# Optimization experiments

Measured on AMD Instinct MI355X. Metric: run time of the kernel, lower is better.

Reference implementation:

```python
import jax, jax.numpy as jnp
import numpy as np
from jax import lax

LATTICE = (16, 16)          # translation-group shape
N_CELLS = 16 * 16           # 256
N_POINT = 8                 # point-group size (e.g. square-lattice C4v)
N_SYMM = N_POINT * N_CELLS  # 2048
FEATURES = 64
IN_FEATURES = 64
BATCH = 64


def setup_inputs() -> dict:
    key = jax.random.key(0)
    k1, k2, k3, k4 = jax.random.split(key, 4)
    x = jax.random.normal(k1, (BATCH, IN_FEATURES, N_SYMM), dtype=jnp.float32)
    kernel = jax.random.normal(k2, (FEATURES, IN_FEATURES, N_SYMM), dtype=jnp.float32) * (
        1.0 / np.sqrt(IN_FEATURES * N_SYMM)
    )
    bias = jax.random.normal(k3, (FEATURES,), dtype=jnp.float32) * 0.02
    product_table = jax.random.randint(k4, (N_POINT, N_SYMM), 0, N_SYMM, dtype=jnp.int64)
    return {"x": x, "kernel": kernel, "bias": bias, "product_table": product_table}


def reference(x, kernel, bias, product_table):
    batch_shape = x.shape[:-2]
    in_features = x.shape[-2]
    # mapping: pt[:n_point] -> (n_point, n_point, *lattice)
    mapping = (
        product_table.reshape(N_POINT, N_CELLS, N_POINT)
        .transpose(0, 2, 1)
        .reshape(N_POINT, N_POINT, *LATTICE)
    )
    # activations: (..., in_f, n_symm) -> (B, in_f, n_point, *lattice)
    xg = x.reshape(-1, in_features, N_CELLS, N_POINT).transpose(0, 1, 3, 2)
    xg = xg.reshape(*xg.shape[:-1], *LATTICE)
    # equivariant kernel via gather: (feat, in_f, n_point, n_point, *lattice)
    kg = kernel[..., mapping]
    # FFT over the translation lattice
    xf = jnp.fft.fftn(xg, s=LATTICE).reshape(*xg.shape[:3], N_CELLS)       # (B,in_f,np,cells)
    kf = jnp.fft.fftn(kg, s=LATTICE).reshape(*kg.shape[:4], N_CELLS)       # (F,in_f,np,np,cells)
    # batched complex contraction over (in_f, n_point), batch over cells
    y = lax.dot_general(xf, kf, (((1, 2), (1, 2)), ((3,), (4,))))          # (cells,B,F,np)
    y = y.transpose(1, 2, 3, 0)                                            # (B,F,np,cells)
    y = y.reshape(*y.shape[:3], *LATTICE)
    y = jnp.fft.ifftn(y, s=LATTICE).reshape(*y.shape[:3], N_CELLS)
    y = y.transpose(0, 1, 3, 2).reshape(*batch_shape, FEATURES, N_SYMM)
    y = y + bias[:, None]
    # input dtype is float32 -> complex result cannot cast back, return real part
    return y.real.astype(jnp.float32)
```

## Files before the change

### kernel.cpp

```cpp
#include <hip/hip_runtime.h>
#include <hip/hip_bf16.h>

typedef __attribute__((ext_vector_type(8))) short bf16x8;
typedef __attribute__((ext_vector_type(16))) float f32x16;
typedef __attribute__((ext_vector_type(2))) float f32x2;
typedef unsigned short ushort_t;

constexpr int NS  = 2048;
constexpr int F   = 64;
constexpr int IFT = 64;
constexpr int B   = 64;
constexpr int NCS = 144;

constexpr float CT[16] = {
    1.0f,  0.9238795325112867f,  0.7071067811865476f,  0.3826834323650898f,
    0.0f, -0.3826834323650898f, -0.7071067811865476f, -0.9238795325112867f,
   -1.0f, -0.9238795325112867f, -0.7071067811865476f, -0.3826834323650898f,
    0.0f,  0.3826834323650898f,  0.7071067811865476f,  0.9238795325112867f};
constexpr float ST[16] = {
    0.0f,  0.3826834323650898f,  0.7071067811865476f,  0.9238795325112867f,
    1.0f,  0.9238795325112867f,  0.7071067811865476f,  0.3826834323650898f,
    0.0f, -0.3826834323650898f, -0.7071067811865476f, -0.9238795325112867f,
   -1.0f, -0.9238795325112867f, -0.7071067811865476f, -0.3826834323650898f};

constexpr int DR4[16] = {0,4,8,12, 1,5,9,13, 2,6,10,14, 3,7,11,15};

template<bool INV>
__device__ inline void dft4(float& ar, float& ai, float& br, float& bi,
                            float& cr, float& ci, float& dr, float& di)
{
    const float t0r = ar + cr, t0i = ai + ci;
    const float t1r = ar - cr, t1i = ai - ci;
    const float t2r = br + dr, t2i = bi + di;
    const float t3r = br - dr, t3i = bi - di;
    ar = t0r + t2r; ai = t0i + t2i;
    cr = t0r - t2r; ci = t0i - t2i;
    if (!INV) { br = t1r + t3i; bi = t1i - t3r; dr = t1r - t3i; di = t1i + t3r; }
    else      { br = t1r - t3i; bi = t1i + t3r; dr = t1r + t3i; di = t1i - t3r; }
}

template<bool INV>
__device__ inline void fft16(float* xr, float* xi)
{
#pragma unroll
    for (int r = 0; r < 4; ++r)
        dft4<INV>(xr[r], xi[r], xr[r + 4], xi[r + 4],
                  xr[r + 8], xi[r + 8], xr[r + 12], xi[r + 12]);
#pragma unroll
    for (int r = 1; r < 4; ++r)
#pragma unroll
        for (int q = 1; q < 4; ++q) {
            const int t = (r * q) & 15;
            const int s = r + 4 * q;
            if (t == 4) {
                const float tr = xr[s];
                if (!INV) { xr[s] = xi[s];  xi[s] = -tr; }
                else      { xr[s] = -xi[s]; xi[s] = tr;  }
            } else {
                const float c = CT[t], sn = INV ? ST[t] : -ST[t];
                const float tr = xr[s];
                xr[s] = tr * c - xi[s] * sn;
                xi[s] = tr * sn + xi[s] * c;
            }
        }
#pragma unroll
    for (int q = 0; q < 4; ++q)
        dft4<INV>(xr[4 * q], xi[4 * q], xr[4 * q + 1], xi[4 * q + 1],
                  xr[4 * q + 2], xi[4 * q + 2], xr[4 * q + 3], xi[4 * q + 3]);
}

template<bool INV>
__device__ inline void dft4c(f32x2& a, f32x2& b, f32x2& c, f32x2& d)
{
    const f32x2 t0 = a + c, t1 = a - c;
    const f32x2 t2 = b + d, t3 = b - d;
    a = t0 + t2; c = t0 - t2;
    f32x2 jt3;
    if (!INV) { jt3.x = t3.y;  jt3.y = -t3.x; }
    else      { jt3.x = -t3.y; jt3.y = t3.x;  }
    b = t1 + jt3; d = t1 - jt3;
}

template<bool INV>
__device__ inline void fft16c(f32x2* z)
{
#pragma unroll
    for (int r = 0; r < 4; ++r) dft4c<INV>(z[r], z[r + 4], z[r + 8], z[r + 12]);
#pragma unroll
    for (int r = 1; r < 4; ++r)
#pragma unroll
        for (int q = 1; q < 4; ++q) {
            const int t = (r * q) & 15, s = r + 4 * q;
            if (t == 4) {
                const f32x2 v = z[s];
                if (!INV) { z[s].x = v.y;  z[s].y = -v.x; }
                else      { z[s].x = -v.y; z[s].y = v.x;  }
            } else {
                const float c = CT[t], sn = INV ? ST[t] : -ST[t];
                const f32x2 v = z[s];
                f32x2 w;
                w.x = v.x * c - v.y * sn;
                w.y = v.x * sn + v.y * c;
                z[s] = w;
            }
        }
#pragma unroll
    for (int q = 0; q < 4; ++q) dft4c<INV>(z[4 * q], z[4 * q + 1], z[4 * q + 2], z[4 * q + 3]);
}

__device__ inline float bf2f(ushort_t h) { return __uint_as_float(((unsigned)h) << 16); }

__device__ inline unsigned pkbf(float a, float b) {
    union { __hip_bfloat162 h2; unsigned u; } c;
    c.h2 = __float22bfloat162_rn(make_float2(a, b));
    return c.u;
}

__device__ inline bf16x8 bneg(bf16x8 v) {
    union { bf16x8 b; unsigned u[4]; } x; x.b = v;
    x.u[0] ^= 0x80008000u; x.u[1] ^= 0x80008000u;
    x.u[2] ^= 0x80008000u; x.u[3] ^= 0x80008000u;
    return x.b;
}

__global__ __launch_bounds__(256) void permute_pt_kernel(
    const int* __restrict__ pt, int* __restrict__ pt2)
{
    const int t = blockIdx.x * 256 + threadIdx.x;
    const int a = t >> 11, r = t & 2047;
    const int bq = r >> 8, s = r & 255;
    pt2[t] = pt[a * NS + s * 8 + bq];
}

__global__ __launch_bounds__(256, 4) void fft_x_kernel(
    const float* __restrict__ x, ushort_t* __restrict__ xf, int i0, int KB)
{
    __shared__ float t_re[16][152], t_im[16][152];
    __shared__ ushort_t stgx[NCS * 68];
    const int tid = threadIdx.x;
    const int bp = blockIdx.x;
    const int il = blockIdx.y;

    const int g = tid >> 4, l = tid & 15;
    const int bloc = g & 1, a = g >> 1;
    const int b = bp * 2 + bloc;
    const int i = i0 + il;

    const float* xr_g = x + ((size_t)b * IFT + i) * NS;
    float xr[16], xi[16];
#pragma unroll
    for (int sx = 0; sx < 16; ++sx) { xr[sx] = xr_g[(l * 16 + sx) * 8 + a]; xi[sx] = 0.f; }
    fft16<false>(xr, xi);
#pragma unroll
    for (int kx = 0; kx < 9; ++kx) {
        t_re[g][kx * 17 + l] = xr[DR4[kx]];
        t_im[g][kx * 17 + l] = xi[DR4[kx]];
    }
    __syncthreads();

    if (l < 9) {
        float Tr[16], Ti[16];
#pragma unroll
        for (int n = 0; n < 16; ++n) { Tr[n] = t_re[g][l * 17 + n]; Ti[n] = t_im[g][l * 17 + n]; }
        fft16<false>(Tr, Ti);
#pragma unroll
        for (int ky = 0; ky < 16; ++ky) {
            const float sr = Tr[DR4[ky]], si = Ti[DR4[ky]];
            const int cs = ky * 9 + l;
            const unsigned w0 = pkbf(sr, si);
            const float rhf = bf2f((ushort_t)(w0 & 0xffffu));
            const float ihf = bf2f((ushort_t)(w0 >> 16));
            const unsigned w1 = pkbf(sr - rhf, si - ihf);
            *(uint2*)&stgx[cs * 68 + bloc * 32 + a * 4] = make_uint2(w0, w1);
        }
    }
    __syncthreads();

    const int kb = il >> 1, mt = bp >> 4;
    const int lb = (il & 1) * 32 + (bp & 15) * 2;
    const size_t PS = (size_t)NCS * 512;
    for (int t = tid; t < NCS * 8; t += 256) {
        const int cs = t >> 3, v4 = (t >> 1) & 3, h = t & 1;
        const int us = ((v4 & 1) << 1) | (v4 >> 1);
        union { ushort_t s[8]; uint4 u; } tmp;
        const int base = cs * 68 + h * 32 + us;
#pragma unroll
        for (int j = 0; j < 8; ++j) tmp.s[j] = stgx[base + j * 4];
        const size_t off = (size_t)(kb * 8 + mt * 4 + v4) * PS + (size_t)cs * 512 + (size_t)(lb + h) * 8;
        *(uint4*)(xf + off) = tmp.u;
    }
}

__global__ __launch_bounds__(256, 4) void fft_k_kernel(
    const float* __restrict__ kern, const int* __restrict__ pt2,
    ushort_t* __restrict__ kf, int i0, int KB)
{
    __shared__ __align__(16) f32x2 t2[16 * 153];
    __shared__ __align__(16) unsigned stgk[NCS * 18];
    f32x2* krow2 = &t2[0];

    const int tid = threadIdx.x;
    const int fg  = blockIdx.x & 15;
    const int bqp = blockIdx.x >> 4;
    const int il  = blockIdx.y;
    const int i   = i0 + il;

    const int g = tid >> 4, l = tid & 15;
    const int bql = g & 1, a = g >> 1;
    const int bq  = bqp * 2 + bql;

    int idx[16];
    const int4* pp = (const int4*)(pt2 + ((a * 8 + bq) * 256 + l * 16));
#pragma unroll
    for (int q = 0; q < 4; ++q) {
        const int4 t4 = pp[q];
        idx[q * 4] = t4.x; idx[q * 4 + 1] = t4.y; idx[q * 4 + 2] = t4.z; idx[q * 4 + 3] = t4.w;
    }

    const int kb = il >> 1;
    const int nt = fg;
    const int pg = (tid * 57) >> 9;
    const int pl = tid - pg * 9;
    const int slot = (pg & 1) * 8 + (pg >> 1);
    const size_t PS = (size_t)NCS * 512;

    for (int p = 0; p < 2; ++p) {
        const int f0 = fg * 4 + p * 2;
        {
            const float4* s0 = (const float4*)(kern + ((size_t)f0 * IFT + i) * NS);
            const float4* s1 = (const float4*)(kern + ((size_t)(f0 + 1) * IFT + i) * NS);
            for (int u = tid; u < 512; u += 256) {
                const float4 va = s0[u], vb = s1[u];
                float4* dst = (float4*)(krow2 + (size_t)u * 4);
                dst[0] = make_float4(va.x, vb.x, va.y, vb.y);
                dst[1] = make_float4(va.z, vb.z, va.w, vb.w);
            }
        }
        __syncthreads();
        f32x2 z[16];
#pragma unroll
        for (int sx = 0; sx < 16; ++sx) z[sx] = krow2[idx[sx]];
        __syncthreads();

        fft16c<false>(z);
        f32x2 F1[9];
#pragma unroll
        for (int kx = 0; kx < 9; ++kx) {
            const f32x2 Zk = z[DR4[kx]];
            const f32x2 Zm = z[DR4[(16 - kx) & 15]];
            f32x2 F0;
            F0.x = (Zk.x + Zm.x) * 0.5f;
            F0.y = (Zk.y - Zm.y) * 0.5f;
            F1[kx].x = (Zk.y + Zm.y) * 0.5f;
            F1[kx].y = (Zm.x - Zk.x) * 0.5f;
            t2[g * 153 + kx * 17 + l] = F0;
        }

        for (int sub = 0; sub < 2; ++sub) {
            if (sub == 1) {
#pragma unroll
                for (int kx = 0; kx < 9; ++kx) t2[g * 153 + kx * 17 + l] = F1[kx];
            }
            __syncthreads();

            if (tid < 144) {
                f32x2 c[16];
#pragma unroll
                for (int n = 0; n < 16; ++n) c[n] = t2[pg * 153 + pl * 17 + n];
                fft16c<false>(c);
#pragma unroll
                for (int ky = 0; ky < 16; ++ky) {
                    const int cs = ky * 9 + pl;
                    const f32x2 v = c[DR4[ky]];
                    stgk[cs * 18 + slot] = pkbf(v.x, v.y);
                }
            }
            __syncthreads();

            const int f = f0 + sub;
            const int lbase = (il & 1) * 32 + (f & 3) * 8 + bqp * 2;
            for (int t = tid; t < NCS * 2; t += 256) {
                const int cs = t >> 1, h = t & 1;
                const int base = cs * 18 + h * 8;
                unsigned w[8];
                *(uint2*)&w[0] = *(const uint2*)&stgk[base];
                *(uint2*)&w[2] = *(const uint2*)&stgk[base + 2];
                *(uint2*)&w[4] = *(const uint2*)&stgk[base + 4];
                *(uint2*)&w[6] = *(const uint2*)&stgk[base + 6];
                union { ushort_t s[8]; uint4 u; } lo, hi;
#pragma unroll
                for (int j = 0; j < 8; ++j) { lo.s[j] = (ushort_t)(w[j] & 0xffffu); hi.s[j] = (ushort_t)(w[j] >> 16); }
                const size_t off = (size_t)(kb * 32 + nt * 2) * PS + (size_t)cs * 512 + (size_t)(lbase + h) * 8;
                *(uint4*)(kf + off) = lo.u;
                *(uint4*)(kf + off + PS) = hi.u;
            }
            __syncthreads();
        }
    }
}

#define MFMA(acc, A, Bv) acc = __builtin_amdgcn_mfma_f32_32x32x16_bf16(A, Bv, acc, 0, 0, 0)
#define LDB(p) (*(const bf16x8*)(p))

__global__ __launch_bounds__(256) void gemm_kernel(
    const ushort_t* __restrict__ xf, const ushort_t* __restrict__ kf,
    float* __restrict__ yre, float* __restrict__ yim, int KB, int acc)
{
    const int cs = blockIdx.x, nb = blockIdx.y;
    const int w = threadIdx.x >> 6, lane = threadIdx.x & 63;
    const int nt = nb * 4 + w;
    const size_t PS = (size_t)NCS * 512;

    f32x16 cre0, cim0, cre1, cim1;
#pragma unroll
    for (int q = 0; q < 16; ++q) { cre0[q] = 0.f; cim0[q] = 0.f; cre1[q] = 0.f; cim1[q] = 0.f; }

    const ushort_t* ab = xf + (size_t)cs * 512 + (size_t)lane * 8;
    const ushort_t* bb = kf + (size_t)cs * 512 + (size_t)(nt * 2) * PS + (size_t)lane * 8;

    const ushort_t* ap = ab;
    const ushort_t* bp = bb;
    bf16x8 Brh = LDB(bp), Bih = LDB(bp + PS);
    bf16x8 Arh0 = LDB(ap), Arl0 = LDB(ap + PS), Aih0 = LDB(ap + 2 * PS), Ail0 = LDB(ap + 3 * PS);
    bf16x8 Arh1 = LDB(ap + 4 * PS), Arl1 = LDB(ap + 5 * PS), Aih1 = LDB(ap + 6 * PS), Ail1 = LDB(ap + 7 * PS);

    for (int kb = 0; kb < KB; ++kb) {
        const int kn = (kb + 1 < KB) ? kb + 1 : kb;
        const ushort_t* an = ab + (size_t)kn * 8 * PS;
        const ushort_t* bn = bb + (size_t)kn * 32 * PS;
        const bf16x8 nBrh = LDB(bn), nBih = LDB(bn + PS);
        const bf16x8 nArh0 = LDB(an), nArl0 = LDB(an + PS), nAih0 = LDB(an + 2 * PS), nAil0 = LDB(an + 3 * PS);
        const bf16x8 nArh1 = LDB(an + 4 * PS), nArl1 = LDB(an + 5 * PS), nAih1 = LDB(an + 6 * PS), nAil1 = LDB(an + 7 * PS);

        const bf16x8 NAih0 = bneg(Aih0), NAil0 = bneg(Ail0);
        const bf16x8 NAih1 = bneg(Aih1), NAil1 = bneg(Ail1);

        MFMA(cre0, Arh0, Brh); MFMA(cre0, Arl0, Brh);
        MFMA(cre0, NAih0, Bih); MFMA(cre0, NAil0, Bih);
        MFMA(cim0, Arh0, Bih); MFMA(cim0, Arl0, Bih);
        MFMA(cim0, Aih0, Brh); MFMA(cim0, Ail0, Brh);
        MFMA(cre1, Arh1, Brh); MFMA(cre1, Arl1, Brh);
        MFMA(cre1, NAih1, Bih); MFMA(cre1, NAil1, Bih);
        MFMA(cim1, Arh1, Bih); MFMA(cim1, Arl1, Bih);
        MFMA(cim1, Aih1, Brh); MFMA(cim1, Ail1, Brh);

        Brh = nBrh; Bih = nBih;
        Arh0 = nArh0; Arl0 = nArl0; Aih0 = nAih0; Ail0 = nAil0;
        Arh1 = nArh1; Arl1 = nArl1; Aih1 = nAih1; Ail1 = nAil1;
    }

    const int col = lane & 31, rhi = (lane >> 5) * 4;
    const int n = nb * 128 + w * 32 + col;
#pragma unroll
    for (int mt = 0; mt < 2; ++mt) {
        const f32x16 cr = mt ? cre1 : cre0;
        const f32x16 ci = mt ? cim1 : cim0;
#pragma unroll
        for (int reg = 0; reg < 16; ++reg) {
            const int row = (reg & 3) + 8 * (reg >> 2) + rhi;
            const size_t off = ((size_t)cs * B + mt * 32 + row) * 512 + n;
            float vr = cr[reg], vi = ci[reg];
            if (acc) { vr += yre[off]; vi += yim[off]; }
            yre[off] = vr; yim[off] = vi;
        }
    }
}

__global__ __launch_bounds__(256, 4) void ifft_y_kernel(
    const float* __restrict__ yre, const float* __restrict__ yim,
    const float* __restrict__ bias, float* __restrict__ out)
{
    __shared__ float yr_s[NCS][17], yi_s[NCS][17];
    __shared__ float t_re[16][271], t_im[16][271];
    __shared__ float ost[2][256][9];
    const int tid = threadIdx.x;
    const int ng = blockIdx.x;
    const int b = blockIdx.y;
    const int n0 = ng * 16;
    for (int t = tid; t < NCS * 16; t += 256) {
        const int cs = t >> 4, nl = t & 15;
        const size_t off = ((size_t)cs * B + b) * 512 + n0 + nl;
        yr_s[cs][nl] = yre[off];
        yi_s[cs][nl] = yim[off];
    }
    __syncthreads();

    const int g = tid >> 4, l = tid & 15;

    float Yr[16], Yi[16];
#pragma unroll
    for (int kx = 0; kx < 16; ++kx) {
        if (kx <= 8) {
            const int cs = l * 9 + kx;
            Yr[kx] = yr_s[cs][g]; Yi[kx] = yi_s[cs][g];
        } else {
            const int cs = ((16 - l) & 15) * 9 + (16 - kx);
            Yr[kx] = yr_s[cs][g]; Yi[kx] = -yi_s[cs][g];
        }
    }
    fft16<true>(Yr, Yi);
#pragma unroll
    for (int sx = 0; sx < 16; ++sx) {
        t_re[g][sx * 17 + l] = Yr[DR4[sx]];
        t_im[g][sx * 17 + l] = Yi[DR4[sx]];
    }
    __syncthreads();

    float Tr[16], Ti[16];
#pragma unroll
    for (int n = 0; n < 16; ++n) { Tr[n] = t_re[g][l * 17 + n]; Ti[n] = t_im[g][l * 17 + n]; }
    fft16<true>(Tr, Ti);
    const int fl = g >> 3, pq = g & 7;
#pragma unroll
    for (int sy = 0; sy < 16; ++sy)
        ost[fl][sy * 16 + l][pq] = Tr[DR4[sy]] * (1.f / 256.f);
    __syncthreads();

    const int f0 = ng * 2;
    for (int t = tid; t < 4096; t += 256) {
        const int flv = t >> 11, e = t & 2047;
        out[((size_t)b * F + f0 + flv) * NS + e] = ost[flv][e >> 3][e & 7] + bias[f0 + flv];
    }
}

extern "C" void kernel_launch(void* const* d_in, const int* in_sizes, int n_in,
                              void* d_out, int out_size, void* d_ws, size_t ws_size,
                              hipStream_t stream)
{
    const float* x = (const float*)d_in[0];
    const float* kern = (const float*)d_in[1];
    const float* bias = (const float*)d_in[2];
    const int* pt = (const int*)d_in[3];
    float* out = (float*)d_out;

    int CI = 2;
    const int cands[6] = {64, 32, 16, 8, 4, 2};
    for (int t = 0; t < 6; ++t) {
        const int KBc = cands[t] / 2;
        const size_t need = 65536
                          + (size_t)NCS * KBc * 8192
                          + (size_t)NCS * KBc * 32768
                          + 2 * (size_t)NCS * B * 512 * 4;
        if (need <= ws_size) { CI = cands[t]; break; }
    }
    const int KB = CI / 2;

    char* p = (char*)d_ws;
    int* pt2 = (int*)p;          p += 65536;
    ushort_t* xf = (ushort_t*)p; p += (size_t)NCS * KB * 8192;
    ushort_t* kf = (ushort_t*)p; p += (size_t)NCS * KB * 32768;
    float* yre = (float*)p;      p += (size_t)NCS * B * 512 * 4;
    float* yim = (float*)p;

    permute_pt_kernel<<<64, 256, 0, stream>>>(pt, pt2);

    const int nch = IFT / CI;
    for (int ch = 0; ch < nch; ++ch) {
        const int i0 = ch * CI;
        fft_x_kernel<<<dim3(32, CI), 256, 0, stream>>>(x, xf, i0, KB);
        fft_k_kernel<<<dim3(64, CI), 256, 0, stream>>>(kern, pt2, kf, i0, KB);
        gemm_kernel<<<dim3(NCS, 4), 256, 0, stream>>>(xf, kf, yre, yim, KB, ch > 0);
    }
    ifft_y_kernel<<<dim3(32, B), 256, 0, stream>>>(yre, yim, bias, out);
}
```

Measured before the change: 288.6 us.

## Restructure kernel-FFT output layout for contiguous 64-byte stores and remap GEMM columns

The kernel-FFT now stages both feature outputs of each pair in shared memory and writes them together, so each pass stores contiguous 64-byte runs per cell instead of scattered 16-byte pieces. This changes the column ordering inside the kf layout, so the GEMM epilogue gets a matching permutation of output column indices. The aim is better global-store coalescing and fewer barrier rounds, at the cost of a larger shared staging buffer.

Result: slower. 309.2 us (+7.1%).

```diff
diff --git a/kernel.cpp b/kernel.cpp
--- a/kernel.cpp
+++ b/kernel.cpp
@@ -196,7 +196,7 @@
     ushort_t* __restrict__ kf, int i0, int KB)
 {
     __shared__ __align__(16) f32x2 t2[16 * 153];
-    __shared__ __align__(16) unsigned stgk[NCS * 18];
+    __shared__ __align__(16) unsigned stgk[NCS * 34];
     f32x2* krow2 = &t2[0];
 
     const int tid = threadIdx.x;
@@ -218,7 +218,6 @@
     }
 
     const int kb = il >> 1;
-    const int nt = fg;
     const int pg = (tid * 57) >> 9;
     const int pl = tid - pg * 9;
     const int slot = (pg & 1) * 8 + (pg >> 1);
@@ -255,47 +254,57 @@
             F1[kx].y = (Zm.x - Zk.x) * 0.5f;
             t2[g * 153 + kx * 17 + l] = F0;
         }
-
-        for (int sub = 0; sub < 2; ++sub) {
-            if (sub == 1) {
-#pragma unroll
-                for (int kx = 0; kx < 9; ++kx) t2[g * 153 + kx * 17 + l] = F1[kx];
+        __syncthreads();
+
+        if (tid < 144) {
+            f32x2 c[16];
+#pragma unroll
+            for (int n = 0; n < 16; ++n) c[n] = t2[pg * 153 + pl * 17 + n];
+            fft16c<false>(c);
+#pragma unroll
+            for (int ky = 0; ky < 16; ++ky) {
+                const int cs = ky * 9 + pl;
+                const f32x2 v = c[DR4[ky]];
+                stgk[cs * 34 + 0 * 16 + slot] = pkbf(v.x, v.y);
             }
-            __syncthreads();
-
-            if (tid < 144) {
-                f32x2 c[16];
-#pragma unroll
-                for (int n = 0; n < 16; ++n) c[n] = t2[pg * 153 + pl * 17 + n];
-                fft16c<false>(c);
-#pragma unroll
-                for (int ky = 0; ky < 16; ++ky) {
-                    const int cs = ky * 9 + pl;
-                    const f32x2 v = c[DR4[ky]];
-                    stgk[cs * 18 + slot] = pkbf(v.x, v.y);
-                }
+        }
+        __syncthreads();
+
+#pragma unroll
+        for (int kx = 0; kx < 9; ++kx) t2[g * 153 + kx * 17 + l] = F1[kx];
+        __syncthreads();
+
+        if (tid < 144) {
+            f32x2 c[16];
+#pragma unroll
+            for (int n = 0; n < 16; ++n) c[n] = t2[pg * 153 + pl * 17 + n];
+            fft16c<false>(c);
+#pragma unroll
+            for (int ky = 0; ky < 16; ++ky) {
+                const int cs = ky * 9 + pl;
+                const f32x2 v = c[DR4[ky]];
+                stgk[cs * 34 + 1 * 16 + slot] = pkbf(v.x, v.y);
             }
-            __syncthreads();
-
-            const int f = f0 + sub;
-            const int lbase = (il & 1) * 32 + (f & 3) * 8 + bqp * 2;
-            for (int t = tid; t < NCS * 2; t += 256) {
-                const int cs = t >> 1, h = t & 1;
-                const int base = cs * 18 + h * 8;
-                unsigned w[8];
-                *(uint2*)&w[0] = *(const uint2*)&stgk[base];
-                *(uint2*)&w[2] = *(const uint2*)&stgk[base + 2];
-                *(uint2*)&w[4] = *(const uint2*)&stgk[base + 4];
-                *(uint2*)&w[6] = *(const uint2*)&stgk[base + 6];
-                union { ushort_t s[8]; uint4 u; } lo, hi;
-#pragma unroll
-                for (int j = 0; j < 8; ++j) { lo.s[j] = (ushort_t)(w[j] & 0xffffu); hi.s[j] = (ushort_t)(w[j] >> 16); }
-                const size_t off = (size_t)(kb * 32 + nt * 2) * PS + (size_t)cs * 512 + (size_t)(lbase + h) * 8;
-                *(uint4*)(kf + off) = lo.u;
-                *(uint4*)(kf + off + PS) = hi.u;
-            }
-            __syncthreads();
-        }
+        }
+        __syncthreads();
+
+        for (int t = tid; t < NCS * 8; t += 256) {
+            const int cs = t >> 3, h = (t >> 2) & 1, c = t & 3;
+            const int base = cs * 34 + (c >> 1) * 16 + (c & 1) * 8;
+            unsigned w[8];
+            *(uint2*)&w[0] = *(const uint2*)&stgk[base];
+            *(uint2*)&w[2] = *(const uint2*)&stgk[base + 2];
+            *(uint2*)&w[4] = *(const uint2*)&stgk[base + 4];
+            *(uint2*)&w[6] = *(const uint2*)&stgk[base + 6];
+            union { ushort_t s[8]; uint4 u; } o;
+#pragma unroll
+            for (int j = 0; j < 8; ++j)
+                o.s[j] = h ? (ushort_t)(w[j] >> 16) : (ushort_t)(w[j] & 0xffffu);
+            const size_t off = (size_t)(kb * 32 + fg * 2 + h) * PS
+                             + (size_t)cs * 512 + (il & 1) * 256 + bqp * 64 + p * 32 + c * 8;
+            *(uint4*)(kf + off) = o.u;
+        }
+        __syncthreads();
     }
 }
 
@@ -350,7 +359,8 @@
     }
 
     const int col = lane & 31, rhi = (lane >> 5) * 4;
-    const int n = nb * 128 + w * 32 + col;
+    const int nact = ((col >> 2) & 1) * 16 + ((col >> 1) & 1) * 8 + ((col >> 3) & 3) * 2 + (col & 1);
+    const int n = nb * 128 + w * 32 + nact;
 #pragma unroll
     for (int mt = 0; mt < 2; ++mt) {
         const f32x16 cr = mt ? cre1 : cre0;
```
